# Kernel tuning notes

Hardware: AMD Instinct MI355X
Metric: run time of the kernel (lower is better)

The kernel has to match this reference:

```python
import jax, jax.numpy as jnp
import numpy as np

N = 8192      # num nodes
D = 128       # feature dim (input_dim)
E = 262144    # num edges (avg degree 32)
P = 4         # num perspectives (num_pers)
EPSILON = 0.3 # similarity threshold (args.epsilon)


def setup_inputs() -> dict:
    key = jax.random.key(0)
    k1, k2, k3, k4 = jax.random.split(key, 4)
    x = jax.random.normal(k1, (N, D), dtype=jnp.float32)
    ori_index = jax.random.randint(k2, (2, E), 0, N, dtype=jnp.int32)
    ori_weight = jax.random.uniform(k3, (E,), dtype=jnp.float32)
    w_pers = jax.random.normal(k4, (P, D), dtype=jnp.float32)  # weighted-cosine perspective weights
    return {"x": x, "ori_index": ori_index, "ori_weight": ori_weight, "w_pers": w_pers}


def reference(x, ori_index, ori_weight, w_pers):
    n = x.shape[0]
    # to_dense_adj: scatter edge weights into dense [N, N] adjacency (duplicate edges add)
    ori_g = jnp.zeros((n, n), dtype=x.dtype).at[ori_index[0], ori_index[1]].add(ori_weight)

    # GraphLearner (weighted multi-perspective cosine):
    # reweight features per perspective, L2-normalize, cosine sim, mean over perspectives
    xw = x[None, :, :] * w_pers[:, None, :]                              # [P, N, D]
    xn = xw / jnp.maximum(jnp.linalg.norm(xw, axis=-1, keepdims=True), 1e-12)
    sim = jnp.mean(jnp.einsum('pnd,pmd->pnm', xn, xn), axis=0)           # [N, N]
    # epsilon-thresholded learned graph
    sim_g = jnp.where(sim > EPSILON, sim, jnp.zeros_like(sim))

    # purified(sim, ori_g, epsilon): keep original edges where sim*ori_g > epsilon
    pur_g = jnp.where(sim * ori_g > EPSILON, ori_g, jnp.zeros_like(sim))
    new_g = pur_g + sim_g
    # dense_to_sparse has data-dependent output size; return the dense refined
    # adjacency (same information: edges = nonzero(new_g), weights = values).
    return new_g
```

## Files before the change

kernel.cpp:

```cpp
#include <hip/hip_runtime.h>
#include <hip/hip_bf16.h>
#include <stdint.h>

#define N_NODES 8192
#define DIM     128
#define KTOT    512
#define NEDGE   262144
#define EPS     0.3f
#define FIX_DELTA 0.0043f
#define HASH_BITS 19
#define HASH_SLOTS (1u << HASH_BITS)
#define NTRI    2080
#define TRI_CAP 376
#define OCAP    131072

typedef unsigned int u32;
typedef unsigned short u16;
typedef __attribute__((ext_vector_type(8))) short short8;
typedef __attribute__((ext_vector_type(4))) float float4v;

#define OFF_YF  0u
#define OFF_YB  16777216u
#define OFF_CTR 25165824u
#define OFF_BC  25166080u
#define OFF_HK  25174528u
#define OFF_HV  27271680u
#define OFF_OL  29368832u
#define OFF_BL  29893120u
#define ZERO_VEC4 262688u

__device__ __forceinline__ u16 f2bf(float f) {
    u32 b = __builtin_bit_cast(u32, f);
    b += 0x7fffu + ((b >> 16) & 1u);
    return (u16)(b >> 16);
}

__device__ __forceinline__ float wave_dot(const float* __restrict__ yf,
                                          u32 i, u32 j, int lane) {
    const float4v* ri = (const float4v*)(yf + (size_t)i * KTOT);
    const float4v* rj = (const float4v*)(yf + (size_t)j * KTOT);
    float4v p = ri[lane] * rj[lane] + ri[64 + lane] * rj[64 + lane];
    float s = p.x + p.y + p.z + p.w;
    #pragma unroll
    for (int o = 32; o >= 1; o >>= 1) s += __shfl_xor(s, o, 64);
    return s;
}

__device__ __forceinline__ u32 tri_of(u32 ti, u32 tj) {
    u32 bm = ti < tj ? ti : tj;
    u32 bn = ti < tj ? tj : ti;
    return bm * (129u - bm) / 2u + (bn - bm);
}

__global__ void prep_y(const float* __restrict__ x, const float* __restrict__ wp,
                       float* __restrict__ yf, u16* __restrict__ yb,
                       uint4* __restrict__ zbase) {
    if (blockIdx.x >= 2048) {
        for (u32 idx = (blockIdx.x - 2048) * 256 + threadIdx.x; idx < ZERO_VEC4;
             idx += 512 * 256)
            zbase[idx] = make_uint4(0, 0, 0, 0);
        return;
    }
    int node = blockIdx.x * 4 + (threadIdx.x >> 6);
    int lane = threadIdx.x & 63;
    float x0 = x[node * DIM + lane];
    float x1 = x[node * DIM + lane + 64];
    for (int p = 0; p < 4; ++p) {
        float v0 = x0 * wp[p * DIM + lane];
        float v1 = x1 * wp[p * DIM + lane + 64];
        float ss = v0 * v0 + v1 * v1;
        #pragma unroll
        for (int o = 1; o < 64; o <<= 1) ss += __shfl_xor(ss, o, 64);
        float scale = 0.5f / fmaxf(sqrtf(ss), 1e-12f);
        float y0 = v0 * scale, y1 = v1 * scale;
        int base = node * KTOT + p * DIM;
        yf[base + lane] = y0;       yf[base + lane + 64] = y1;
        yb[base + lane] = f2bf(y0); yb[base + lane + 64] = f2bf(y1);
    }
}

__global__ void edge_insert(const int* __restrict__ idx, const float* __restrict__ w,
                            u32* __restrict__ hkey, float* __restrict__ hval,
                            u32* __restrict__ bcnt, u32* __restrict__ blist,
                            u32* __restrict__ ocnt, u32* __restrict__ olist) {
    int e = blockIdx.x * 256 + threadIdx.x;
    u32 i = (u32)idx[e], j = (u32)idx[NEDGE + e];
    u32 cell = i * (u32)N_NODES + j;
    float wv = w[e];
    u32 key = cell + 1u;
    u32 h = (cell * 2654435761u) >> (32 - HASH_BITS);
    while (true) {
        u32 old = atomicCAS(&hkey[h], 0u, key);
        if (old == 0u) {
            u32 tri = tri_of(i >> 7, j >> 7);
            u32 bi = atomicAdd(&bcnt[tri], 1u);
            if (bi < TRI_CAP) blist[tri * TRI_CAP + bi] = h;
            else { u32 g = atomicAdd(ocnt, 1u); if (g < OCAP) olist[g] = h; }
            atomicAdd(&hval[h], wv);
            break;
        }
        if (old == key) { atomicAdd(&hval[h], wv); break; }
        h = (h + 1u) & (HASH_SLOTS - 1u);
    }
}

#define TM  128
#define BK  64
#define TLD 132

__global__ __launch_bounds__(512)
void gemm_sim(const u16* __restrict__ yb, const float* __restrict__ yf,
              float* __restrict__ out,
              const u32* __restrict__ hkey, const float* __restrict__ hval,
              const u32* __restrict__ bcnt, const u32* __restrict__ blist,
              const u32* __restrict__ ocnt, const u32* __restrict__ olist) {
    int r = blockIdx.y, c = blockIdx.x;
    int bm, bn;
    if (c < 64 - r) { bm = r;      bn = r + c; }
    else            { bm = 63 - r; bn = bm + (c - (64 - r)); }
    __shared__ __align__(16) char smem[64 * TLD * 4];
    u16* As = (u16*)smem;
    u16* Bs = As + TM * BK;
    float* tbuf = (float*)smem;
    int tid = threadIdx.x;
    int lane = tid & 63, wid = tid >> 6;
    int wm = wid >> 1, wn = wid & 1;

    float4v acc[2][4] = {};
    const u16* arow = yb + (size_t)(bm * TM) * KTOT;
    const u16* brow = yb + (size_t)(bn * TM) * KTOT;

    for (int kt = 0; kt < KTOT / BK; ++kt) {
        __syncthreads();
        #pragma unroll
        for (int q = 0; q < 2; ++q) {
            int cc = q * 512 + wid * 64 + lane;
            int row = cc >> 3;
            int kg = (cc & 7) ^ (row & 7);
            __builtin_amdgcn_global_load_lds(
                (const __attribute__((address_space(1))) void*)(const void*)(arow + (size_t)row * KTOT + kt * BK + kg * 8),
                (__attribute__((address_space(3))) void*)(void*)(As + (q * 512 + wid * 64) * 8),
                16, 0, 0);
            __builtin_amdgcn_global_load_lds(
                (const __attribute__((address_space(1))) void*)(const void*)(brow + (size_t)row * KTOT + kt * BK + kg * 8),
                (__attribute__((address_space(3))) void*)(void*)(Bs + (q * 512 + wid * 64) * 8),
                16, 0, 0);
        }
        __syncthreads();
        #pragma unroll
        for (int kk = 0; kk < 2; ++kk) {
            short8 af[2], bfr[4];
            int kg2 = kk * 4 + (lane >> 4);
            int mrow = wm * 32 + (lane & 15);
            int ncol = wn * 64 + (lane & 15);
            #pragma unroll
            for (int i = 0; i < 2; ++i) {
                int ra = mrow + i * 16;
                af[i] = *(const short8*)&As[ra * BK + ((kg2 ^ (ra & 7)) * 8)];
            }
            #pragma unroll
            for (int j = 0; j < 4; ++j) {
                int rb = ncol + j * 16;
                bfr[j] = *(const short8*)&Bs[rb * BK + ((kg2 ^ (rb & 7)) * 8)];
            }
            #pragma unroll
            for (int i = 0; i < 2; ++i)
                #pragma unroll
                for (int j = 0; j < 4; ++j)
                    acc[i][j] = __builtin_amdgcn_mfma_f32_16x16x32_bf16(
                        af[i], bfr[j], acc[i][j], 0, 0, 0);
        }
    }

    int quad = lane >> 4, lcol = lane & 15;
    #pragma unroll
    for (int i = 0; i < 2; ++i)
        #pragma unroll
        for (int j = 0; j < 4; ++j) {
            int gr0 = bm * TM + wm * 32 + i * 16 + quad * 4;
            int gc  = bn * TM + wn * 64 + j * 16 + lcol;
            #pragma unroll
            for (int rr = 0; rr < 4; ++rr) {
                float s = acc[i][j][rr];
                __builtin_nontemporal_store(s > EPS ? s : 0.f,
                                            &out[(size_t)(gr0 + rr) * N_NODES + gc]);
            }
        }

    #pragma unroll
    for (int h = 0; h < 2; ++h) {
        __syncthreads();
        if (wn == h) {
            #pragma unroll
            for (int i = 0; i < 2; ++i) {
                int Lr = wm * 32 + i * 16 + quad * 4;
                #pragma unroll
                for (int j = 0; j < 4; ++j) {
                    int Lc = j * 16 + lcol;
                    *(float4v*)&tbuf[Lc * TLD + Lr] = acc[i][j];
                }
            }
        }
        __syncthreads();
        #pragma unroll
        for (int v = 0; v < 4; ++v) {
            int chunk = v * 512 + tid;
            int row = chunk >> 5, c4 = chunk & 31;
            float4v t = *(const float4v*)&tbuf[row * TLD + c4 * 4];
            float4v o;
            #pragma unroll
            for (int rr = 0; rr < 4; ++rr) o[rr] = t[rr] > EPS ? t[rr] : 0.f;
            __builtin_nontemporal_store(o,
                (float4v*)&out[(size_t)(bn * TM + h * 64 + row) * N_NODES + bm * TM + c4 * 4]);
        }
    }

    __syncthreads();

    #pragma unroll
    for (int i = 0; i < 2; ++i)
        #pragma unroll
        for (int j = 0; j < 4; ++j)
            #pragma unroll
            for (int rr = 0; rr < 4; ++rr) {
                float s = acc[i][j][rr];
                unsigned long long m = __ballot(fabsf(s - EPS) < FIX_DELTA);
                while (m) {
                    int src = __builtin_ctzll(m);
                    m &= m - 1;
                    u32 ii = (u32)(bm * TM + wm * 32 + i * 16 + (src >> 4) * 4 + rr);
                    u32 jj = (u32)(bn * TM + wn * 64 + j * 16 + (src & 15));
                    float sx = wave_dot(yf, ii, jj, lane);
                    if (lane == 0) {
                        float v = sx > EPS ? sx : 0.f;
                        out[(size_t)ii * N_NODES + jj] = v;
                        out[(size_t)jj * N_NODES + ii] = v;
                    }
                }
            }

    __syncthreads();

    u32 tri = tri_of((u32)bm, (u32)bn);
    u32 cnt = bcnt[tri]; if (cnt > TRI_CAP) cnt = TRI_CAP;
    {
        u32 t = (u32)tid;
        bool valid = t < cnt;
        u32 cell = 0; float a = 0.f, sg = 0.f; bool hardc = false;
        if (valid) {
            u32 h = blist[tri * TRI_CAP + t];
            cell = hkey[h] - 1u;
            a = hval[h];
            sg = out[cell];
            hardc = (a > 1.0f) ||
                    (fabsf(sg - EPS) < FIX_DELTA + 1e-6f) ||
                    (sg > 0.f && fabsf(sg * a - EPS) < FIX_DELTA * a + 1e-6f) ||
                    (sg == 0.f && a > 0.9855f);
            if (!hardc && sg > 0.f)
                out[cell] = sg + ((sg * a > EPS) ? a : 0.f);
        }
        unsigned long long m = __ballot(hardc);
        while (m) {
            int src = __builtin_ctzll(m);
            m &= m - 1;
            u32 cB = __shfl(cell, src, 64);
            float aB = __shfl(a, src, 64);
            float sx = wave_dot(yf, cB >> 13, cB & 8191u, lane);
            if (lane == 0) {
                float v = sx > EPS ? sx : 0.f;
                if (sx * aB > EPS) v += aB;
                out[cB] = v;
            }
        }
    }

    u32 ovn = *ocnt; if (ovn > OCAP) ovn = OCAP;
    for (u32 base = 0; base < ovn; base += 512) {
        u32 t = base + (u32)tid;
        bool valid = t < ovn;
        u32 cell = 0; float a = 0.f, sg = 0.f; bool hardc = false;
        if (valid) {
            u32 h = olist[t];
            cell = hkey[h] - 1u;
            u32 ii = cell >> 13, jj = cell & 8191u;
            if (tri_of(ii >> 7, jj >> 7) == tri) {
                a = hval[h];
                sg = out[cell];
                hardc = (a > 1.0f) ||
                        (fabsf(sg - EPS) < FIX_DELTA + 1e-6f) ||
                        (sg > 0.f && fabsf(sg * a - EPS) < FIX_DELTA * a + 1e-6f) ||
                        (sg == 0.f && a > 0.9855f);
                if (!hardc && sg > 0.f)
                    out[cell] = sg + ((sg * a > EPS) ? a : 0.f);
            }
        }
        unsigned long long m = __ballot(hardc);
        while (m) {
            int src = __builtin_ctzll(m);
            m &= m - 1;
            u32 cB = __shfl(cell, src, 64);
            float aB = __shfl(a, src, 64);
            float sx = wave_dot(yf, cB >> 13, cB & 8191u, lane);
            if (lane == 0) {
                float v = sx > EPS ? sx : 0.f;
                if (sx * aB > EPS) v += aB;
                out[cB] = v;
            }
        }
    }
}

extern "C" void kernel_launch(void* const* d_in, const int* in_sizes, int n_in,
                              void* d_out, int out_size, void* d_ws, size_t ws_size,
                              hipStream_t stream) {
    const float* x  = (const float*)d_in[0];
    const int*   oi = (const int*)d_in[1];
    const float* ow = (const float*)d_in[2];
    const float* wp = (const float*)d_in[3];
    float* out = (float*)d_out;
    char* ws = (char*)d_ws;
    float* yf = (float*)(ws + OFF_YF);
    u16*   yb = (u16*)(ws + OFF_YB);
    u32*   oc = (u32*)(ws + OFF_CTR);
    u32*   bc = (u32*)(ws + OFF_BC);
    u32*   hk = (u32*)(ws + OFF_HK);
    float* hv = (float*)(ws + OFF_HV);
    u32*   ol = (u32*)(ws + OFF_OL);
    u32*   bl = (u32*)(ws + OFF_BL);

    prep_y<<<2560, 256, 0, stream>>>(x, wp, yf, yb, (uint4*)(ws + OFF_CTR));
    edge_insert<<<NEDGE / 256, 256, 0, stream>>>(oi, ow, hk, hv, bc, bl, oc, ol);
    gemm_sim<<<dim3(65, 32), 512, 0, stream>>>(yb, yf, out, hk, hv, bc, bl, oc, ol);
}
```

Baseline: 429.0 us.

## Pre-zero output in prep kernel and write only above-threshold sims sparsely

Adds 8192 blocks to the prep kernel that zero the whole 256MB dense output with nontemporal vector stores. The GEMM epilogue then writes only entries above epsilon, as scattered scalar stores to both (i,j) and (j,i), and drops the LDS transpose buffer. The aim is to replace the dense thresholded writes with one streaming zero fill plus a few sparse writes. The risks are that the zero fill still moves the full output, and that the scattered transposed stores are uncoalesced.

```diff
diff --git a/kernel.cpp b/kernel.cpp
--- a/kernel.cpp
+++ b/kernel.cpp
@@ -18,6 +18,7 @@
 typedef unsigned short u16;
 typedef __attribute__((ext_vector_type(8))) short short8;
 typedef __attribute__((ext_vector_type(4))) float float4v;
+typedef __attribute__((ext_vector_type(4))) u32 u32x4;
 
 #define OFF_YF  0u
 #define OFF_YB  16777216u
@@ -29,6 +30,8 @@
 #define OFF_BL  29893120u
 #define ZERO_VEC4 262688u
 
+#define OZBLK   8192u
+
 __device__ __forceinline__ u16 f2bf(float f) {
     u32 b = __builtin_bit_cast(u32, f);
     b += 0x7fffu + ((b >> 16) & 1u);
@@ -54,11 +57,20 @@
 
 __global__ void prep_y(const float* __restrict__ x, const float* __restrict__ wp,
                        float* __restrict__ yf, u16* __restrict__ yb,
-                       uint4* __restrict__ zbase) {
+                       u32x4* __restrict__ zbase, u32x4* __restrict__ outv) {
+    if (blockIdx.x >= 2560) {
+        u32 t = (blockIdx.x - 2560) * 256 + threadIdx.x;
+        u32x4 z = {0u, 0u, 0u, 0u};
+        #pragma unroll
+        for (u32 q = 0; q < 8; ++q)
+            __builtin_nontemporal_store(z, &outv[(size_t)q * (OZBLK * 256u) + t]);
+        return;
+    }
     if (blockIdx.x >= 2048) {
+        u32x4 z = {0u, 0u, 0u, 0u};
         for (u32 idx = (blockIdx.x - 2048) * 256 + threadIdx.x; idx < ZERO_VEC4;
              idx += 512 * 256)
-            zbase[idx] = make_uint4(0, 0, 0, 0);
+            zbase[idx] = z;
         return;
     }
     int node = blockIdx.x * 4 + (threadIdx.x >> 6);
@@ -106,7 +118,6 @@
 
 #define TM  128
 #define BK  64
-#define TLD 132
 
 __global__ __launch_bounds__(512)
 void gemm_sim(const u16* __restrict__ yb, const float* __restrict__ yf,
@@ -118,10 +129,8 @@
     int bm, bn;
     if (c < 64 - r) { bm = r;      bn = r + c; }
     else            { bm = 63 - r; bn = bm + (c - (64 - r)); }
-    __shared__ __align__(16) char smem[64 * TLD * 4];
-    u16* As = (u16*)smem;
-    u16* Bs = As + TM * BK;
-    float* tbuf = (float*)smem;
+    __shared__ __align__(16) u16 As[TM * BK];
+    __shared__ __align__(16) u16 Bs[TM * BK];
     int tid = threadIdx.x;
     int lane = tid & 63, wid = tid >> 6;
     int wm = wid >> 1, wn = wid & 1;
@@ -176,65 +185,30 @@
     #pragma unroll
     for (int i = 0; i < 2; ++i)
         #pragma unroll
-        for (int j = 0; j < 4; ++j) {
-            int gr0 = bm * TM + wm * 32 + i * 16 + quad * 4;
-            int gc  = bn * TM + wn * 64 + j * 16 + lcol;
-            #pragma unroll
-            for (int rr = 0; rr < 4; ++rr) {
-                float s = acc[i][j][rr];
-                __builtin_nontemporal_store(s > EPS ? s : 0.f,
-                                            &out[(size_t)(gr0 + rr) * N_NODES + gc]);
-            }
-        }
-
-    #pragma unroll
-    for (int h = 0; h < 2; ++h) {
-        __syncthreads();
-        if (wn == h) {
-            #pragma unroll
-            for (int i = 0; i < 2; ++i) {
-                int Lr = wm * 32 + i * 16 + quad * 4;
-                #pragma unroll
-                for (int j = 0; j < 4; ++j) {
-                    int Lc = j * 16 + lcol;
-                    *(float4v*)&tbuf[Lc * TLD + Lr] = acc[i][j];
-                }
-            }
-        }
-        __syncthreads();
-        #pragma unroll
-        for (int v = 0; v < 4; ++v) {
-            int chunk = v * 512 + tid;
-            int row = chunk >> 5, c4 = chunk & 31;
-            float4v t = *(const float4v*)&tbuf[row * TLD + c4 * 4];
-            float4v o;
-            #pragma unroll
-            for (int rr = 0; rr < 4; ++rr) o[rr] = t[rr] > EPS ? t[rr] : 0.f;
-            __builtin_nontemporal_store(o,
-                (float4v*)&out[(size_t)(bn * TM + h * 64 + row) * N_NODES + bm * TM + c4 * 4]);
-        }
-    }
-
-    __syncthreads();
-
-    #pragma unroll
-    for (int i = 0; i < 2; ++i)
-        #pragma unroll
         for (int j = 0; j < 4; ++j)
             #pragma unroll
             for (int rr = 0; rr < 4; ++rr) {
                 float s = acc[i][j][rr];
-                unsigned long long m = __ballot(fabsf(s - EPS) < FIX_DELTA);
+                u32 ii = (u32)(bm * TM + wm * 32 + i * 16 + quad * 4 + rr);
+                u32 jj = (u32)(bn * TM + wn * 64 + j * 16 + lcol);
+                bool knife = fabsf(s - EPS) < FIX_DELTA;
+                if (!knife && s > EPS) {
+                    __builtin_nontemporal_store(s, &out[(size_t)ii * N_NODES + jj]);
+                    __builtin_nontemporal_store(s, &out[(size_t)jj * N_NODES + ii]);
+                }
+                unsigned long long m = __ballot(knife);
                 while (m) {
                     int src = __builtin_ctzll(m);
                     m &= m - 1;
-                    u32 ii = (u32)(bm * TM + wm * 32 + i * 16 + (src >> 4) * 4 + rr);
-                    u32 jj = (u32)(bn * TM + wn * 64 + j * 16 + (src & 15));
-                    float sx = wave_dot(yf, ii, jj, lane);
+                    u32 fi = (u32)(bm * TM + wm * 32 + i * 16 + (src >> 4) * 4 + rr);
+                    u32 fj = (u32)(bn * TM + wn * 64 + j * 16 + (src & 15));
+                    float sx = wave_dot(yf, fi, fj, lane);
                     if (lane == 0) {
                         float v = sx > EPS ? sx : 0.f;
-                        out[(size_t)ii * N_NODES + jj] = v;
-                        out[(size_t)jj * N_NODES + ii] = v;
+                        if (v != 0.f) {
+                            out[(size_t)fi * N_NODES + fj] = v;
+                            out[(size_t)fj * N_NODES + fi] = v;
+                        }
                     }
                 }
             }
@@ -328,7 +302,8 @@
     u32*   ol = (u32*)(ws + OFF_OL);
     u32*   bl = (u32*)(ws + OFF_BL);
 
-    prep_y<<<2560, 256, 0, stream>>>(x, wp, yf, yb, (uint4*)(ws + OFF_CTR));
+    prep_y<<<2560 + OZBLK, 256, 0, stream>>>(x, wp, yf, yb,
+                                             (u32x4*)(ws + OFF_CTR), (u32x4*)out);
     edge_insert<<<NEDGE / 256, 256, 0, stream>>>(oi, ow, hk, hv, bc, bl, oc, ol);
     gemm_sim<<<dim3(65, 32), 512, 0, stream>>>(yb, yf, out, hk, hv, bc, bl, oc, ol);
 }
```

Measured after the change: 442.4 us. +3.1%, slower.
